# Kernel optimization log

Measured on AMD Instinct MI355X. Metric: run time of the kernel, lower is better.

## Reference

```python
import jax, jax.numpy as jnp
import numpy as np

D_MODEL, N_HEADS, WINDOW, N_STATE = 1024, 16, 256, 128
B, T = 2, 2048
EPS = 1e-5


def _layernorm(x, g, b):
    mu = jnp.mean(x, axis=-1, keepdims=True)
    var = jnp.mean((x - mu) ** 2, axis=-1, keepdims=True)
    return (x - mu) * jax.lax.rsqrt(var + EPS) * g + b


def setup_inputs() -> dict:
    key = jax.random.key(0)
    ks = jax.random.split(key, 20)
    d, h = D_MODEL, 4 * D_MODEL
    s = lambda k, *shape: jax.random.normal(k, shape, jnp.float32) * 0.02
    return {
        "x": jax.random.normal(ks[0], (B, T, d), jnp.float32),
        "ssm_state": jnp.zeros((B, N_STATE), jnp.float32),
        "ln1_g": jnp.ones((d,), jnp.float32), "ln1_b": jnp.zeros((d,), jnp.float32),
        "wq": s(ks[1], d, d), "bq": jnp.zeros((d,), jnp.float32),
        "wk": s(ks[2], d, d), "bk": jnp.zeros((d,), jnp.float32),
        "wv": s(ks[3], d, d), "bv": jnp.zeros((d,), jnp.float32),
        "wo": s(ks[4], d, d), "bo": jnp.zeros((d,), jnp.float32),
        "wg": s(ks[5], d, d), "bg": jnp.zeros((d,), jnp.float32),
        "A": jax.random.uniform(ks[6], (N_STATE,), jnp.float32, -0.1, 0.1),
        "Bw": s(ks[7], d, N_STATE),
        "Cw": s(ks[8], N_STATE, d),
        "ln2_g": jnp.ones((d,), jnp.float32), "ln2_b": jnp.zeros((d,), jnp.float32),
        "w1": s(ks[9], d, h), "b1": jnp.zeros((h,), jnp.float32),
        "w2": s(ks[10], h, d), "b2": jnp.zeros((d,), jnp.float32),
    }


def _forward(x, ssm_state, ln1_g, ln1_b, wq, bq, wk, bk, wv, bv, wo, bo,
             wg, bg, A, Bw, Cw, ln2_g, ln2_b, w1, b1, w2, b2):
    Bsz, Tlen, d = x.shape
    d_h = d // N_HEADS
    xn = _layernorm(x, ln1_g, ln1_b)

    # --- windowed causal attention (dense, per original) ---
    def heads(y):
        return y.reshape(Bsz, Tlen, N_HEADS, d_h).transpose(0, 2, 1, 3)
    Q = heads(xn @ wq + bq)
    K = heads(xn @ wk + bk)
    V = heads(xn @ wv + bv)
    scores = jnp.einsum("bhqd,bhkd->bhqk", Q, K) / (d_h ** 0.5)
    i = jnp.arange(Tlen)[:, None]
    j = jnp.arange(Tlen)[None, :]
    allowed = (j <= i) & (i - j < WINDOW)
    scores = jnp.where(allowed, scores, -jnp.inf)
    attn = jax.nn.softmax(scores, axis=-1)
    ao = jnp.einsum("bhqk,bhkd->bhqd", attn, V)
    ao = ao.transpose(0, 2, 1, 3).reshape(Bsz, Tlen, d)
    attn_out = ao @ wo + bo

    # --- diagonal SSM scan ---
    u = xn @ Bw  # (B,T,N)
    def step(s, u_t):
        s = A * s + u_t
        return s, s
    new_state, states = jax.lax.scan(step, ssm_state, u.transpose(1, 0, 2))
    ssm_out = states.transpose(1, 0, 2) @ Cw  # (B,T,d)

    # --- gated fusion + residual + MLP ---
    g = jax.nn.sigmoid(xn @ wg + bg)
    x = x + g * attn_out + (1.0 - g) * ssm_out
    xn2 = _layernorm(x, ln2_g, ln2_b)
    mlp = jax.nn.gelu(xn2 @ w1 + b1, approximate=False) @ w2 + b2
    return x + mlp, new_state


def reference(x, ssm_state, ln1_g, ln1_b, wq, bq, wk, bk, wv, bv, wo, bo,
              wg, bg, A, Bw, Cw, ln2_g, ln2_b, w1, b1, w2, b2):
    return _forward(x, ssm_state, ln1_g, ln1_b, wq, bq, wk, bk, wv, bv, wo, bo,
                    wg, bg, A, Bw, Cw, ln2_g, ln2_b, w1, b1, w2, b2)
```

## Files before the change

kernel.cpp:

```cpp
#include <hip/hip_runtime.h>

typedef __attribute__((ext_vector_type(8))) short bf16x8;
typedef __attribute__((ext_vector_type(4))) float f32x4;

#define D_MODEL 1024
#define T_LEN 2048
#define BATCH 2
#define N_HEADS 16
#define D_HEAD 64
#define WINDOW 256
#define N_STATE 128
#define D_FF 4096
#define N_CAT 4224
#define LDQ 4352
#define M_ROWS 4096

static __device__ __forceinline__ float bf2f(unsigned short u) {
  union { unsigned int i; float f; } v; v.i = ((unsigned int)u) << 16; return v.f;
}
static __device__ __forceinline__ unsigned short f2bf(float f) {
  unsigned int x = __float_as_uint(f);
  return (unsigned short)((x + 0x7FFFu + ((x >> 16) & 1u)) >> 16);
}

static __device__ __forceinline__ void gl_lds16(const void* g, void* l) {
  __builtin_amdgcn_global_load_lds(
      (const __attribute__((address_space(1))) unsigned int*)g,
      (__attribute__((address_space(3))) unsigned int*)l, 16, 0, 0);
}

__global__ __launch_bounds__(256) void transpose_cvt(
    const float* __restrict__ src, unsigned short* __restrict__ dst,
    int K, int N, int n_off, int ldd)
{
  __shared__ float tile[32][33];
  const int kt = blockIdx.x * 32, nt = blockIdx.y * 32;
  const int c = threadIdx.x & 31, r0 = threadIdx.x >> 5;
#pragma unroll
  for (int i = 0; i < 4; i++) {
    const int r = r0 + i * 8;
    tile[r][c] = src[(size_t)(kt + r) * N + nt + c];
  }
  __syncthreads();
#pragma unroll
  for (int i = 0; i < 4; i++) {
    const int r = r0 + i * 8;
    dst[(size_t)(n_off + nt + r) * ldd + kt + c] = f2bf(tile[c][r]);
  }
}

__global__ __launch_bounds__(256) void transpose5(
    const float* __restrict__ s0, const float* __restrict__ s1,
    const float* __restrict__ s2, const float* __restrict__ s3,
    const float* __restrict__ s4, unsigned short* __restrict__ dcat,
    unsigned short* __restrict__ dwo)
{
  __shared__ float tile[32][33];
  const int z = blockIdx.z;
  const float* src = (z == 0) ? s0 : (z == 1) ? s1 : (z == 2) ? s2 : (z == 3) ? s3 : s4;
  unsigned short* dst = (z < 4) ? dcat + (size_t)z * 1024 * 1024 : dwo;
  const int kt = blockIdx.x * 32, nt = blockIdx.y * 32;
  const int c = threadIdx.x & 31, r0 = threadIdx.x >> 5;
#pragma unroll
  for (int i = 0; i < 4; i++) {
    const int r = r0 + i * 8;
    tile[r][c] = src[(size_t)(kt + r) * 1024 + nt + c];
  }
  __syncthreads();
#pragma unroll
  for (int i = 0; i < 4; i++) {
    const int r = r0 + i * 8;
    dst[(size_t)(nt + r) * 1024 + kt + c] = f2bf(tile[c][r]);
  }
}

__global__ __launch_bounds__(256) void vtrans_kernel(
    const unsigned short* __restrict__ qkvgu, unsigned short* __restrict__ VT)
{
  __shared__ unsigned short tile[32][33];
  const int bh = blockIdx.z;
  const int b = bh >> 4, h = bh & 15;
  const int t0 = blockIdx.x * 32, d0 = blockIdx.y * 32;
  const int c = threadIdx.x & 31, r0 = threadIdx.x >> 5;
#pragma unroll
  for (int i = 0; i < 4; i++) {
    const int r = r0 + i * 8;
    tile[r][c] = qkvgu[((size_t)b * T_LEN + t0 + r) * LDQ + 2048 + h * 64 + d0 + c];
  }
  __syncthreads();
#pragma unroll
  for (int i = 0; i < 4; i++) {
    const int r = r0 + i * 8;
    VT[((size_t)bh * 64 + d0 + r) * T_LEN + t0 + c] = tile[c][r];
  }
}

__global__ __launch_bounds__(256) void build_bcat(
    const float* __restrict__ bq, const float* __restrict__ bk,
    const float* __restrict__ bv, const float* __restrict__ bg,
    float* __restrict__ bcat)
{
  const int i = blockIdx.x * 256 + threadIdx.x;
  if (i < LDQ) {
    float v = 0.0f;
    if (i < 1024)      v = bq[i];
    else if (i < 2048) v = bk[i - 1024];
    else if (i < 3072) v = bv[i - 2048];
    else if (i < 4096) v = bg[i - 3072];
    bcat[i] = v;
  }
}

__global__ __launch_bounds__(256) void ln_kernel(
    const float* __restrict__ x, const float* __restrict__ g,
    const float* __restrict__ b, unsigned short* __restrict__ out)
{
  const int row = blockIdx.x, tid = threadIdx.x;
  const float4 xv = ((const float4*)(x + (size_t)row * 1024))[tid];
  float s  = xv.x + xv.y + xv.z + xv.w;
  float s2 = xv.x * xv.x + xv.y * xv.y + xv.z * xv.z + xv.w * xv.w;
#pragma unroll
  for (int off = 32; off >= 1; off >>= 1) {
    s  += __shfl_down(s, off);
    s2 += __shfl_down(s2, off);
  }
  __shared__ float red[8];
  const int wave = tid >> 6;
  if ((tid & 63) == 0) { red[wave] = s; red[4 + wave] = s2; }
  __syncthreads();
  s  = red[0] + red[1] + red[2] + red[3];
  s2 = red[4] + red[5] + red[6] + red[7];
  const float mu = s * (1.0f / 1024.0f);
  const float rs = rsqrtf(s2 * (1.0f / 1024.0f) - mu * mu + 1e-5f);
  const float4 gv = ((const float4*)g)[tid];
  const float4 bv = ((const float4*)b)[tid];
  ushort4 o;
  o.x = f2bf((xv.x - mu) * rs * gv.x + bv.x);
  o.y = f2bf((xv.y - mu) * rs * gv.y + bv.y);
  o.z = f2bf((xv.z - mu) * rs * gv.z + bv.z);
  o.w = f2bf((xv.w - mu) * rs * gv.w + bv.w);
  ((ushort4*)(out + (size_t)row * 1024))[tid] = o;
}

template<int ACT>
__global__ __launch_bounds__(256, 3) void gemm128ho(
    const unsigned short* __restrict__ A, const unsigned short* __restrict__ BT,
    const float* __restrict__ bias, unsigned short* __restrict__ C,
    int ldc, int K, int nby)
{
  __shared__ char smem[32768];
  char* const As = smem;
  char* const Bs = smem + 16384;
  const int nwg = gridDim.x;
  int bid = blockIdx.x;
  {
    const int q = nwg >> 3, r = nwg & 7, xx = bid & 7, o = bid >> 3;
    bid = (xx < r ? xx * (q + 1) : r * (q + 1) + (xx - r) * q) + o;
  }
  const int per_group = 8 * nby;
  const int grp = bid / per_group, rem = bid % per_group;
  const int m0 = (grp * 8 + (rem & 7)) * 128;
  const int n0 = (rem >> 3) * 128;

  const int tid = threadIdx.x, lane = tid & 63, wave = tid >> 6;
  const int l15 = lane & 15, lg = lane >> 4;
  const int wm = (wave >> 1) * 64, wn = (wave & 1) * 64;
  f32x4 acc[4][4];
#pragma unroll
  for (int i = 0; i < 4; i++)
#pragma unroll
    for (int j = 0; j < 4; j++) acc[i][j] = (f32x4){0.f, 0.f, 0.f, 0.f};

  const char* srcA[4]; const char* srcB[4];
#pragma unroll
  for (int j = 0; j < 4; j++) {
    const int p = j * 4096 + tid * 16;
    const int R = p >> 7;
    const int cb = (p & 127) ^ ((R & 7) << 4);
    srcA[j] = (const char*)A  + (size_t)(m0 + R) * (size_t)(K * 2) + cb;
    srcB[j] = (const char*)BT + (size_t)(n0 + R) * (size_t)(K * 2) + cb;
  }

  const int NT = K >> 6;
  for (int t = 0; t < NT; ++t) {
    __syncthreads();
#pragma unroll
    for (int j = 0; j < 4; j++) {
      gl_lds16(srcA[j] + (size_t)t * 128, As + j * 4096 + tid * 16);
      gl_lds16(srcB[j] + (size_t)t * 128, Bs + j * 4096 + tid * 16);
    }
    __syncthreads();
    bf16x8 af[4][2], bfr[4][2];
#pragma unroll
    for (int mf = 0; mf < 4; mf++)
#pragma unroll
      for (int ks = 0; ks < 2; ks++) {
        const int R = wm + mf * 16 + l15;
        af[mf][ks] = *(const bf16x8*)(As + (R << 7) + ((ks * 64 + lg * 16) ^ ((R & 7) << 4)));
      }
#pragma unroll
    for (int nf = 0; nf < 4; nf++)
#pragma unroll
      for (int ks = 0; ks < 2; ks++) {
        const int R = wn + nf * 16 + l15;
        bfr[nf][ks] = *(const bf16x8*)(Bs + (R << 7) + ((ks * 64 + lg * 16) ^ ((R & 7) << 4)));
      }
#pragma unroll
    for (int mf = 0; mf < 4; mf++)
#pragma unroll
      for (int nf = 0; nf < 4; nf++)
#pragma unroll
        for (int ks = 0; ks < 2; ks++)
          acc[mf][nf] = __builtin_amdgcn_mfma_f32_16x16x32_bf16(
              af[mf][ks], bfr[nf][ks], acc[mf][nf], 0, 0, 0);
  }

  __syncthreads();
  unsigned short (*Ct)[128] = (unsigned short(*)[128])smem;
#pragma unroll
  for (int nf = 0; nf < 4; nf++) {
    const int col = wn + nf * 16 + l15;
    const float bv = bias[n0 + col];
#pragma unroll
    for (int mf = 0; mf < 4; mf++) {
      const int rbase = wm + mf * 16 + lg * 4;
#pragma unroll
      for (int r = 0; r < 4; r++) {
        float v = acc[mf][nf][r] + bv;
        if (ACT == 2) v = 0.5f * v * (1.0f + erff(v * 0.70710678118654752f));
        Ct[rbase + r][col] = f2bf(v);
      }
    }
  }
  __syncthreads();
#pragma unroll
  for (int pass = 0; pass < 8; pass++) {
    const int idx = pass * 256 + tid;
    const int row = idx >> 4, c8 = (idx & 15) * 8;
    const uint4 d = *(const uint4*)&Ct[row][c8];
    *(uint4*)(C + (size_t)(m0 + row) * ldc + n0 + c8) = d;
  }
}

template<int ACT, bool OUT_BF16, bool RESID>
__global__ __launch_bounds__(256, 4) void gemm_ho(
    const unsigned short* __restrict__ A, const unsigned short* __restrict__ BT,
    const float* __restrict__ bias, const float* __restrict__ resid,
    void* __restrict__ Cout, int ldc, int K, int nbx)
{
  __shared__ char As[16384];
  __shared__ char Bs[8192];
  const int nwg = gridDim.x;
  int bid = blockIdx.x;
  {
    const int q = nwg >> 3, r = nwg & 7, xx = bid & 7, o = bid >> 3;
    bid = (xx < r ? xx * (q + 1) : r * (q + 1) + (xx - r) * q) + o;
  }
  const int m0 = (bid % nbx) * 128;
  const int n0 = (bid / nbx) * 64;
  const int tid = threadIdx.x, lane = tid & 63, wave = tid >> 6;
  const int l15 = lane & 15, lg = lane >> 4;
  const int wm = (wave & 1) * 64, wn = (wave >> 1) * 32;
  f32x4 acc[4][2];
#pragma unroll
  for (int i = 0; i < 4; i++)
#pragma unroll
    for (int j = 0; j < 2; j++) acc[i][j] = (f32x4){0.f, 0.f, 0.f, 0.f};

  const char* srcA[4]; const char* srcB[2];
#pragma unroll
  for (int j = 0; j < 4; j++) {
    const int p = j * 4096 + tid * 16;
    const int R = p >> 7;
    const int cb = (p & 127) ^ ((R & 7) << 4);
    srcA[j] = (const char*)A + (size_t)(m0 + R) * (size_t)(K * 2) + cb;
    if (j < 2) srcB[j] = (const char*)BT + (size_t)(n0 + R) * (size_t)(K * 2) + cb;
  }

  const int NT = K >> 6;
  for (int t = 0; t < NT; ++t) {
    __syncthreads();
#pragma unroll
    for (int j = 0; j < 4; j++)
      gl_lds16(srcA[j] + (size_t)t * 128, As + j * 4096 + tid * 16);
#pragma unroll
    for (int j = 0; j < 2; j++)
      gl_lds16(srcB[j] + (size_t)t * 128, Bs + j * 4096 + tid * 16);
    __syncthreads();
    bf16x8 af[4][2], bfr[2][2];
#pragma unroll
    for (int mf = 0; mf < 4; mf++)
#pragma unroll
      for (int ks = 0; ks < 2; ks++) {
        const int R = wm + mf * 16 + l15;
        af[mf][ks] = *(const bf16x8*)(As + (R << 7) + ((ks * 64 + lg * 16) ^ ((R & 7) << 4)));
      }
#pragma unroll
    for (int nf = 0; nf < 2; nf++)
#pragma unroll
      for (int ks = 0; ks < 2; ks++) {
        const int R = wn + nf * 16 + l15;
        bfr[nf][ks] = *(const bf16x8*)(Bs + (R << 7) + ((ks * 64 + lg * 16) ^ ((R & 7) << 4)));
      }
#pragma unroll
    for (int mf = 0; mf < 4; mf++)
#pragma unroll
      for (int nf = 0; nf < 2; nf++)
#pragma unroll
        for (int ks = 0; ks < 2; ks++)
          acc[mf][nf] = __builtin_amdgcn_mfma_f32_16x16x32_bf16(
              af[mf][ks], bfr[nf][ks], acc[mf][nf], 0, 0, 0);
  }

  if (OUT_BF16) {
    __syncthreads();
    unsigned short (*Ct)[64] = (unsigned short(*)[64])As;
#pragma unroll
    for (int nf = 0; nf < 2; nf++) {
      const int col = wn + nf * 16 + l15;
      const float bv = bias ? bias[n0 + col] : 0.0f;
#pragma unroll
      for (int mf = 0; mf < 4; mf++) {
        const int rbase = wm + mf * 16 + lg * 4;
#pragma unroll
        for (int r = 0; r < 4; r++) {
          float v = acc[mf][nf][r] + bv;
          if (ACT == 2) v = 0.5f * v * (1.0f + erff(v * 0.70710678118654752f));
          Ct[rbase + r][col] = f2bf(v);
        }
      }
    }
    __syncthreads();
    unsigned short* Cb = (unsigned short*)Cout;
#pragma unroll
    for (int pass = 0; pass < 4; pass++) {
      const int idx = pass * 256 + tid;
      const int row = idx >> 3, c8 = (idx & 7) * 8;
      const uint4 d = *(const uint4*)&Ct[row][c8];
      *(uint4*)(Cb + (size_t)(m0 + row) * ldc + n0 + c8) = d;
    }
  } else {
#pragma unroll
    for (int nf = 0; nf < 2; nf++) {
      const int col = n0 + wn + nf * 16 + l15;
      const float bv = bias ? bias[col] : 0.0f;
#pragma unroll
      for (int mf = 0; mf < 4; mf++) {
        const int rbase = m0 + wm + mf * 16 + lg * 4;
#pragma unroll
        for (int r = 0; r < 4; r++) {
          float v = acc[mf][nf][r] + bv;
          if (ACT == 2) v = 0.5f * v * (1.0f + erff(v * 0.70710678118654752f));
          const size_t idx = (size_t)(rbase + r) * ldc + col;
          if (RESID) v += resid[idx];
          ((float*)Cout)[idx] = v;
        }
      }
    }
  }
}

__global__ __launch_bounds__(256) void attn_kernel(
    const unsigned short* __restrict__ qkvgu, const unsigned short* __restrict__ VT,
    unsigned short* __restrict__ ao)
{
  __shared__ float S[16][276];
  unsigned short* P = (unsigned short*)&S[0][0];

  const int bx = ((blockIdx.x & 7) << 4) | (blockIdx.x >> 3);
  const int q0 = bx * 16;
  const int h  = blockIdx.y;
  const int b  = blockIdx.z;
  const int tid = threadIdx.x, lane = tid & 63, wave = tid >> 6;
  const int l15 = lane & 15, lg = lane >> 4;
  const size_t rowbase = (size_t)b * T_LEN;

  {
    const unsigned short* qp = qkvgu + (rowbase + q0 + l15) * LDQ + h * 64 + lg * 8;
    const bf16x8 aq0 = *(const bf16x8*)qp;
    const bf16x8 aq1 = *(const bf16x8*)(qp + 32);
    for (int kt = wave; kt < 17; kt += 4) {
      const int kbase = q0 - 256 + kt * 16;
      const int krow = kbase + l15;
      const int krc = krow < 0 ? 0 : krow;
      const unsigned short* kp = qkvgu + (rowbase + krc) * LDQ + 1024 + h * 64 + lg * 8;
      const bf16x8 bk0 = *(const bf16x8*)kp;
      const bf16x8 bk1 = *(const bf16x8*)(kp + 32);
      f32x4 sacc = (f32x4){0.f, 0.f, 0.f, 0.f};
      sacc = __builtin_amdgcn_mfma_f32_16x16x32_bf16(aq0, bk0, sacc, 0, 0, 0);
      sacc = __builtin_amdgcn_mfma_f32_16x16x32_bf16(aq1, bk1, sacc, 0, 0, 0);
#pragma unroll
      for (int r = 0; r < 4; r++) {
        const int qi = q0 + lg * 4 + r;
        const int kj = kbase + l15;
        const bool ok = (kj >= 0) && (kj <= qi) && (qi - kj < WINDOW);
        S[lg * 4 + r][kt * 16 + l15] = ok ? sacc[r] * 0.125f : -1e30f;
      }
    }
  }
  __syncthreads();

  {
    const int q = tid >> 4, sub = tid & 15;
    float mx = -1e30f;
    for (int c = sub; c < 272; c += 16) mx = fmaxf(mx, S[q][c]);
#pragma unroll
    for (int off = 8; off >= 1; off >>= 1) mx = fmaxf(mx, __shfl_xor(mx, off));
    float sum = 0.f;
    for (int c = sub; c < 272; c += 16) sum += __expf(S[q][c] - mx);
#pragma unroll
    for (int off = 8; off >= 1; off >>= 1) sum += __shfl_xor(sum, off);
    const float inv = 1.0f / sum;
    unsigned short* Prow = P + q * 552;
    for (int c = sub; c < 288; c += 16) {
      const float pv = (c < 272) ? __expf(S[q][c] - mx) * inv : 0.0f;
      Prow[c] = f2bf(pv);
    }
  }
  __syncthreads();

  {
    f32x4 oacc = (f32x4){0.f, 0.f, 0.f, 0.f};
    const int dn = wave * 16 + l15;
    const unsigned short* vrow = VT + ((size_t)(b * 16 + h) * 64 + dn) * T_LEN;
#pragma unroll
    for (int ks = 0; ks < 9; ks++) {
      const bf16x8 pa = *(const bf16x8*)(P + l15 * 552 + ks * 32 + lg * 8);
      int t = q0 - 256 + ks * 32 + lg * 8;
      t = t < 0 ? 0 : (t > T_LEN - 8 ? T_LEN - 8 : t);
      const bf16x8 vb = *(const bf16x8*)(vrow + t);
      oacc = __builtin_amdgcn_mfma_f32_16x16x32_bf16(pa, vb, oacc, 0, 0, 0);
    }
#pragma unroll
    for (int r = 0; r < 4; r++)
      ao[(rowbase + q0 + lg * 4 + r) * D_MODEL + h * 64 + dn] = f2bf(oacc[r]);
  }
}

__global__ __launch_bounds__(1024) void scan_kernel(
    const unsigned short* __restrict__ qkvgu, const float* __restrict__ Avec,
    const float* __restrict__ s0, unsigned short* __restrict__ states,
    float* __restrict__ out_state)
{
  __shared__ float finals[16][128];
  const int b = blockIdx.x;
  const int tid = threadIdx.x;
  const int c = tid >> 6;
  const int n0 = (tid & 63) * 2;
  const float a0 = Avec[n0], a1 = Avec[n0 + 1];
  float sv0 = (c == 0) ? s0[b * 128 + n0]     : 0.0f;
  float sv1 = (c == 0) ? s0[b * 128 + n0 + 1] : 0.0f;
  const size_t ubase = (size_t)b * T_LEN * LDQ + 4096 + n0;
  unsigned short* sp = states + (size_t)b * T_LEN * N_STATE + n0;
  const int t0 = c * 128;
#pragma unroll 8
  for (int t = t0; t < t0 + 128; t++) {
    const ushort2 u = *(const ushort2*)&qkvgu[ubase + (size_t)t * LDQ];
    sv0 = fmaf(a0, sv0, bf2f(u.x));
    sv1 = fmaf(a1, sv1, bf2f(u.y));
    ushort2 o; o.x = f2bf(sv0); o.y = f2bf(sv1);
    *(ushort2*)&sp[(size_t)t * N_STATE] = o;
  }
  finals[c][n0] = sv0;
  finals[c][n0 + 1] = sv1;
  if (c == 15) { out_state[b * 128 + n0] = sv0; out_state[b * 128 + n0 + 1] = sv1; }
  __syncthreads();
  if (c > 0) {
    const float c0 = finals[c - 1][n0];
    const float c1 = finals[c - 1][n0 + 1];
    float f0 = a0, f1 = a1;
    for (int t = t0; t < t0 + 128; t++) {
      if (f0 == 0.0f && f1 == 0.0f) break;
      ushort2 cur = *(ushort2*)&sp[(size_t)t * N_STATE];
      cur.x = f2bf(bf2f(cur.x) + f0 * c0);
      cur.y = f2bf(bf2f(cur.y) + f1 * c1);
      *(ushort2*)&sp[(size_t)t * N_STATE] = cur;
      f0 *= a0; f1 *= a1;
    }
  }
}

__global__ __launch_bounds__(256) void fusion_ln2_kernel(
    const float* __restrict__ x, const unsigned short* __restrict__ qkvgu,
    const unsigned short* __restrict__ attn, const unsigned short* __restrict__ ssm,
    const float* __restrict__ g2, const float* __restrict__ b2,
    float* __restrict__ out, unsigned short* __restrict__ xn2)
{
  const int row = blockIdx.x, tid = threadIdx.x;
  const size_t e4 = (size_t)row * 1024 + tid * 4;
  const float4 xv = *(const float4*)(x + e4);
  const ushort4 au = *(const ushort4*)(attn + e4);
  const ushort4 su = *(const ushort4*)(ssm + e4);
  const ushort4 gu = *(const ushort4*)(qkvgu + (size_t)row * LDQ + 3072 + tid * 4);
  float4 o;
  {
    const float ga = 1.0f / (1.0f + __expf(-bf2f(gu.x)));
    const float gb = 1.0f / (1.0f + __expf(-bf2f(gu.y)));
    const float gc = 1.0f / (1.0f + __expf(-bf2f(gu.z)));
    const float gd = 1.0f / (1.0f + __expf(-bf2f(gu.w)));
    o.x = xv.x + ga * bf2f(au.x) + (1.0f - ga) * bf2f(su.x);
    o.y = xv.y + gb * bf2f(au.y) + (1.0f - gb) * bf2f(su.y);
    o.z = xv.z + gc * bf2f(au.z) + (1.0f - gc) * bf2f(su.z);
    o.w = xv.w + gd * bf2f(au.w) + (1.0f - gd) * bf2f(su.w);
  }
  *(float4*)(out + e4) = o;

  float s  = o.x + o.y + o.z + o.w;
  float s2 = o.x * o.x + o.y * o.y + o.z * o.z + o.w * o.w;
#pragma unroll
  for (int off = 32; off >= 1; off >>= 1) {
    s  += __shfl_down(s, off);
    s2 += __shfl_down(s2, off);
  }
  __shared__ float red[8];
  const int wave = tid >> 6;
  if ((tid & 63) == 0) { red[wave] = s; red[4 + wave] = s2; }
  __syncthreads();
  s  = red[0] + red[1] + red[2] + red[3];
  s2 = red[4] + red[5] + red[6] + red[7];
  const float mu = s * (1.0f / 1024.0f);
  const float rs = rsqrtf(s2 * (1.0f / 1024.0f) - mu * mu + 1e-5f);
  const float4 gv = ((const float4*)g2)[tid];
  const float4 bv = ((const float4*)b2)[tid];
  ushort4 ov;
  ov.x = f2bf((o.x - mu) * rs * gv.x + bv.x);
  ov.y = f2bf((o.y - mu) * rs * gv.y + bv.y);
  ov.z = f2bf((o.z - mu) * rs * gv.z + bv.z);
  ov.w = f2bf((o.w - mu) * rs * gv.w + bv.w);
  ((ushort4*)(xn2 + (size_t)row * 1024))[tid] = ov;
}

extern "C" void kernel_launch(void* const* d_in, const int* in_sizes, int n_in,
                              void* d_out, int out_size, void* d_ws, size_t ws_size,
                              hipStream_t stream)
{
  const float* x     = (const float*)d_in[0];
  const float* ssm0  = (const float*)d_in[1];
  const float* ln1_g = (const float*)d_in[2];
  const float* ln1_b = (const float*)d_in[3];
  const float* wq    = (const float*)d_in[4];
  const float* bq    = (const float*)d_in[5];
  const float* wk    = (const float*)d_in[6];
  const float* bk    = (const float*)d_in[7];
  const float* wv    = (const float*)d_in[8];
  const float* bv    = (const float*)d_in[9];
  const float* wo    = (const float*)d_in[10];
  const float* bo    = (const float*)d_in[11];
  const float* wg    = (const float*)d_in[12];
  const float* bg    = (const float*)d_in[13];
  const float* Av    = (const float*)d_in[14];
  const float* Bw    = (const float*)d_in[15];
  const float* Cw    = (const float*)d_in[16];
  const float* ln2_g = (const float*)d_in[17];
  const float* ln2_b = (const float*)d_in[18];
  const float* w1    = (const float*)d_in[19];
  const float* b1    = (const float*)d_in[20];
  const float* w2    = (const float*)d_in[21];
  const float* b2    = (const float*)d_in[22];

  char* p = (char*)d_ws;
  auto take = [&](size_t bytes) { char* q = p; p += (bytes + 255) & ~(size_t)255; return q; };
  unsigned short* WcatT  = (unsigned short*)take((size_t)LDQ * 1024 * 2);
  unsigned short* woT    = (unsigned short*)take((size_t)1024 * 1024 * 2);
  unsigned short* CwT    = (unsigned short*)take((size_t)1024 * 128 * 2);
  unsigned short* w1T    = (unsigned short*)take((size_t)4096 * 1024 * 2);
  unsigned short* w2T    = (unsigned short*)take((size_t)1024 * 4096 * 2);
  float*          bcat   = (float*)take((size_t)LDQ * 4);
  unsigned short* xn     = (unsigned short*)take((size_t)M_ROWS * 1024 * 2);
  unsigned short* qkvgu  = (unsigned short*)take((size_t)M_ROWS * LDQ * 2);
  unsigned short* VT     = (unsigned short*)take((size_t)BATCH * N_HEADS * 64 * T_LEN * 2);
  unsigned short* ao     = (unsigned short*)take((size_t)M_ROWS * 1024 * 2);
  unsigned short* states = (unsigned short*)take((size_t)M_ROWS * N_STATE * 2);
  unsigned short* attn_o = (unsigned short*)take((size_t)M_ROWS * 1024 * 2);
  unsigned short* ssm_o  = (unsigned short*)take((size_t)M_ROWS * 1024 * 2);
  unsigned short* hbuf   = qkvgu;

  float* outx = (float*)d_out;
  float* out_state = outx + (size_t)M_ROWS * 1024;

  transpose5<<<dim3(32, 32, 5), 256, 0, stream>>>(wq, wk, wv, wg, wo, WcatT, woT);
  transpose_cvt<<<dim3(32, 4), 256, 0, stream>>>(Bw, WcatT, 1024, 128, 4096, 1024);
  transpose_cvt<<<dim3(4, 32), 256, 0, stream>>>(Cw, CwT, 128, 1024, 0, 128);
  transpose_cvt<<<dim3(32, 128), 256, 0, stream>>>(w1, w1T, 1024, 4096, 0, 1024);
  transpose_cvt<<<dim3(128, 32), 256, 0, stream>>>(w2, w2T, 4096, 1024, 0, 4096);
  build_bcat<<<17, 256, 0, stream>>>(bq, bk, bv, bg, bcat);

  ln_kernel<<<M_ROWS, 256, 0, stream>>>(x, ln1_g, ln1_b, xn);
  gemm128ho<0><<<32 * 34, 256, 0, stream>>>(xn, WcatT, bcat, qkvgu, LDQ, 1024, 34);
  vtrans_kernel<<<dim3(64, 2, 32), 256, 0, stream>>>(qkvgu, VT);
  attn_kernel<<<dim3(128, 16, 2), 256, 0, stream>>>(qkvgu, VT, ao);
  scan_kernel<<<2, 1024, 0, stream>>>(qkvgu, Av, ssm0, states, out_state);
  gemm_ho<0, true, false><<<32 * 16, 256, 0, stream>>>(
      ao, woT, bo, nullptr, attn_o, 1024, 1024, 32);
  gemm_ho<0, true, false><<<32 * 16, 256, 0, stream>>>(
      states, CwT, nullptr, nullptr, ssm_o, 1024, 128, 32);
  fusion_ln2_kernel<<<4096, 256, 0, stream>>>(
      x, qkvgu, attn_o, ssm_o, ln2_g, ln2_b, outx, xn);
  gemm128ho<2><<<32 * 32, 256, 0, stream>>>(xn, w1T, b1, hbuf, 4096, 1024, 32);
  gemm_ho<0, false, true><<<32 * 16, 256, 0, stream>>>(
      hbuf, w2T, b2, outx, outx, 1024, 4096, 32);
}
```

Measured before the change: 307.7 us.

## Merge prep kernels, fold scan into attention launch, dual-job output GEMM

Replaces the six weight-transpose and bias-concat launches with a single prep kernel indexed by a flat block id. Folds the SSM scan into extra blocks of the attention launch, using four 512-step chunks per batch instead of sixteen 128-step chunks, so it overlaps with attention. Replaces the two separate output-projection and Cw GEMMs with one launch using 128x64 tiles that serves both jobs. Also raises the occupancy hint of gemm128ho. Fewer launches and more concurrency are the goal, but the scan now has a longer serial chain per thread and occupies only two blocks.

```diff
diff --git a/kernel.cpp b/kernel.cpp
--- a/kernel.cpp
+++ b/kernel.cpp
@@ -29,12 +29,55 @@
       (__attribute__((address_space(3))) unsigned int*)l, 16, 0, 0);
 }
 
-__global__ __launch_bounds__(256) void transpose_cvt(
-    const float* __restrict__ src, unsigned short* __restrict__ dst,
-    int K, int N, int n_off, int ldd)
-{
+__global__ __launch_bounds__(256) void prep_kernel(
+    const float* __restrict__ wq, const float* __restrict__ wk,
+    const float* __restrict__ wv, const float* __restrict__ wg,
+    const float* __restrict__ wo, const float* __restrict__ Bw,
+    const float* __restrict__ Cw, const float* __restrict__ w1,
+    const float* __restrict__ w2,
+    const float* __restrict__ bq, const float* __restrict__ bk,
+    const float* __restrict__ bv, const float* __restrict__ bg,
+    unsigned short* __restrict__ WcatT, unsigned short* __restrict__ woT,
+    unsigned short* __restrict__ CwT, unsigned short* __restrict__ w1T,
+    unsigned short* __restrict__ w2T, float* __restrict__ bcat)
+{
+  const int bid = blockIdx.x;
+  if (bid >= 13568) {
+    const int i = (bid - 13568) * 256 + threadIdx.x;
+    if (i < LDQ) {
+      float v = 0.0f;
+      if (i < 1024)      v = bq[i];
+      else if (i < 2048) v = bk[i - 1024];
+      else if (i < 3072) v = bv[i - 2048];
+      else if (i < 4096) v = bg[i - 3072];
+      bcat[i] = v;
+    }
+    return;
+  }
+  const float* src; unsigned short* dst;
+  int N, n_off, ldd, x, y;
+  if (bid < 5120) {
+    const int z = bid >> 10, t = bid & 1023;
+    x = t & 31; y = t >> 5;
+    src = (z == 0) ? wq : (z == 1) ? wk : (z == 2) ? wv : (z == 3) ? wg : wo;
+    dst = (z < 4) ? WcatT : woT;
+    n_off = (z < 4) ? z * 1024 : 0;
+    N = 1024; ldd = 1024;
+  } else if (bid < 5248) {
+    const int t = bid - 5120; x = t & 31; y = t >> 5;
+    src = Bw; dst = WcatT; n_off = 4096; N = 128; ldd = 1024;
+  } else if (bid < 5376) {
+    const int t = bid - 5248; x = t & 3; y = t >> 2;
+    src = Cw; dst = CwT; n_off = 0; N = 1024; ldd = 128;
+  } else if (bid < 9472) {
+    const int t = bid - 5376; x = t & 31; y = t >> 5;
+    src = w1; dst = w1T; n_off = 0; N = 4096; ldd = 1024;
+  } else {
+    const int t = bid - 9472; x = t & 127; y = t >> 7;
+    src = w2; dst = w2T; n_off = 0; N = 1024; ldd = 4096;
+  }
   __shared__ float tile[32][33];
-  const int kt = blockIdx.x * 32, nt = blockIdx.y * 32;
+  const int kt = x * 32, nt = y * 32;
   const int c = threadIdx.x & 31, r0 = threadIdx.x >> 5;
 #pragma unroll
   for (int i = 0; i < 4; i++) {
@@ -46,31 +89,6 @@
   for (int i = 0; i < 4; i++) {
     const int r = r0 + i * 8;
     dst[(size_t)(n_off + nt + r) * ldd + kt + c] = f2bf(tile[c][r]);
-  }
-}
-
-__global__ __launch_bounds__(256) void transpose5(
-    const float* __restrict__ s0, const float* __restrict__ s1,
-    const float* __restrict__ s2, const float* __restrict__ s3,
-    const float* __restrict__ s4, unsigned short* __restrict__ dcat,
-    unsigned short* __restrict__ dwo)
-{
-  __shared__ float tile[32][33];
-  const int z = blockIdx.z;
-  const float* src = (z == 0) ? s0 : (z == 1) ? s1 : (z == 2) ? s2 : (z == 3) ? s3 : s4;
-  unsigned short* dst = (z < 4) ? dcat + (size_t)z * 1024 * 1024 : dwo;
-  const int kt = blockIdx.x * 32, nt = blockIdx.y * 32;
-  const int c = threadIdx.x & 31, r0 = threadIdx.x >> 5;
-#pragma unroll
-  for (int i = 0; i < 4; i++) {
-    const int r = r0 + i * 8;
-    tile[r][c] = src[(size_t)(kt + r) * 1024 + nt + c];
-  }
-  __syncthreads();
-#pragma unroll
-  for (int i = 0; i < 4; i++) {
-    const int r = r0 + i * 8;
-    dst[(size_t)(nt + r) * 1024 + kt + c] = f2bf(tile[c][r]);
   }
 }
 
@@ -92,22 +110,6 @@
   for (int i = 0; i < 4; i++) {
     const int r = r0 + i * 8;
     VT[((size_t)bh * 64 + d0 + r) * T_LEN + t0 + c] = tile[c][r];
-  }
-}
-
-__global__ __launch_bounds__(256) void build_bcat(
-    const float* __restrict__ bq, const float* __restrict__ bk,
-    const float* __restrict__ bv, const float* __restrict__ bg,
-    float* __restrict__ bcat)
-{
-  const int i = blockIdx.x * 256 + threadIdx.x;
-  if (i < LDQ) {
-    float v = 0.0f;
-    if (i < 1024)      v = bq[i];
-    else if (i < 2048) v = bk[i - 1024];
-    else if (i < 3072) v = bv[i - 2048];
-    else if (i < 4096) v = bg[i - 3072];
-    bcat[i] = v;
   }
 }
 
@@ -143,7 +145,7 @@
 }
 
 template<int ACT>
-__global__ __launch_bounds__(256, 3) void gemm128ho(
+__global__ __launch_bounds__(256, 4) void gemm128ho(
     const unsigned short* __restrict__ A, const unsigned short* __restrict__ BT,
     const float* __restrict__ bias, unsigned short* __restrict__ C,
     int ldc, int K, int nby)
@@ -360,18 +362,164 @@
   }
 }
 
-__global__ __launch_bounds__(256) void attn_kernel(
+__global__ __launch_bounds__(256, 4) void gemm_dual(
+    const unsigned short* __restrict__ A1, const unsigned short* __restrict__ BT1,
+    const float* __restrict__ bias1, unsigned short* __restrict__ C1, int K1,
+    const unsigned short* __restrict__ A2, const unsigned short* __restrict__ BT2,
+    const float* __restrict__ bias2, unsigned short* __restrict__ C2, int K2)
+{
+  __shared__ char As[16384];
+  __shared__ char Bs[8192];
+  const int nwg = gridDim.x;
+  int bid = blockIdx.x;
+  {
+    const int q = nwg >> 3, r = nwg & 7, xx = bid & 7, o = bid >> 3;
+    bid = (xx < r ? xx * (q + 1) : r * (q + 1) + (xx - r) * q) + o;
+  }
+  const int job = bid >> 9;
+  const int inner = bid & 511;
+  const unsigned short* A  = job ? A2 : A1;
+  const unsigned short* BT = job ? BT2 : BT1;
+  const float* bias        = job ? bias2 : bias1;
+  unsigned short* C        = job ? C2 : C1;
+  const int K              = job ? K2 : K1;
+  const int m0 = (inner & 31) * 128;
+  const int n0 = (inner >> 5) * 64;
+  const int ldc = 1024;
+
+  const int tid = threadIdx.x, lane = tid & 63, wave = tid >> 6;
+  const int l15 = lane & 15, lg = lane >> 4;
+  const int wm = (wave & 1) * 64, wn = (wave >> 1) * 32;
+  f32x4 acc[4][2];
+#pragma unroll
+  for (int i = 0; i < 4; i++)
+#pragma unroll
+    for (int j = 0; j < 2; j++) acc[i][j] = (f32x4){0.f, 0.f, 0.f, 0.f};
+
+  const char* srcA[4]; const char* srcB[2];
+#pragma unroll
+  for (int j = 0; j < 4; j++) {
+    const int p = j * 4096 + tid * 16;
+    const int R = p >> 7;
+    const int cb = (p & 127) ^ ((R & 7) << 4);
+    srcA[j] = (const char*)A + (size_t)(m0 + R) * (size_t)(K * 2) + cb;
+    if (j < 2) srcB[j] = (const char*)BT + (size_t)(n0 + R) * (size_t)(K * 2) + cb;
+  }
+
+  const int NT = K >> 6;
+  for (int t = 0; t < NT; ++t) {
+    __syncthreads();
+#pragma unroll
+    for (int j = 0; j < 4; j++)
+      gl_lds16(srcA[j] + (size_t)t * 128, As + j * 4096 + tid * 16);
+#pragma unroll
+    for (int j = 0; j < 2; j++)
+      gl_lds16(srcB[j] + (size_t)t * 128, Bs + j * 4096 + tid * 16);
+    __syncthreads();
+    bf16x8 af[4][2], bfr[2][2];
+#pragma unroll
+    for (int mf = 0; mf < 4; mf++)
+#pragma unroll
+      for (int ks = 0; ks < 2; ks++) {
+        const int R = wm + mf * 16 + l15;
+        af[mf][ks] = *(const bf16x8*)(As + (R << 7) + ((ks * 64 + lg * 16) ^ ((R & 7) << 4)));
+      }
+#pragma unroll
+    for (int nf = 0; nf < 2; nf++)
+#pragma unroll
+      for (int ks = 0; ks < 2; ks++) {
+        const int R = wn + nf * 16 + l15;
+        bfr[nf][ks] = *(const bf16x8*)(Bs + (R << 7) + ((ks * 64 + lg * 16) ^ ((R & 7) << 4)));
+      }
+#pragma unroll
+    for (int mf = 0; mf < 4; mf++)
+#pragma unroll
+      for (int nf = 0; nf < 2; nf++)
+#pragma unroll
+        for (int ks = 0; ks < 2; ks++)
+          acc[mf][nf] = __builtin_amdgcn_mfma_f32_16x16x32_bf16(
+              af[mf][ks], bfr[nf][ks], acc[mf][nf], 0, 0, 0);
+  }
+
+  __syncthreads();
+  unsigned short (*Ct)[64] = (unsigned short(*)[64])As;
+#pragma unroll
+  for (int nf = 0; nf < 2; nf++) {
+    const int col = wn + nf * 16 + l15;
+    const float bv = bias ? bias[n0 + col] : 0.0f;
+#pragma unroll
+    for (int mf = 0; mf < 4; mf++) {
+      const int rbase = wm + mf * 16 + lg * 4;
+#pragma unroll
+      for (int r = 0; r < 4; r++)
+        Ct[rbase + r][col] = f2bf(acc[mf][nf][r] + bv);
+    }
+  }
+  __syncthreads();
+#pragma unroll
+  for (int pass = 0; pass < 4; pass++) {
+    const int idx = pass * 256 + tid;
+    const int row = idx >> 3, c8 = (idx & 7) * 8;
+    const uint4 d = *(const uint4*)&Ct[row][c8];
+    *(uint4*)(C + (size_t)(m0 + row) * ldc + n0 + c8) = d;
+  }
+}
+
+__global__ __launch_bounds__(256) void attn_scan_kernel(
     const unsigned short* __restrict__ qkvgu, const unsigned short* __restrict__ VT,
-    unsigned short* __restrict__ ao)
+    unsigned short* __restrict__ ao, const float* __restrict__ Avec,
+    const float* __restrict__ s0, unsigned short* __restrict__ states,
+    float* __restrict__ out_state)
 {
   __shared__ float S[16][276];
+  const int tid = threadIdx.x;
+
+  if (blockIdx.x >= 128) {
+    if (blockIdx.y != 0 || blockIdx.z != 0 || blockIdx.x > 129) return;
+    float (*finals)[128] = (float(*)[128])&S[0][0];
+    const int b = blockIdx.x - 128;
+    const int c = tid >> 6;
+    const int n0 = (tid & 63) * 2;
+    const float a0 = Avec[n0], a1 = Avec[n0 + 1];
+    float sv0 = (c == 0) ? s0[b * 128 + n0]     : 0.0f;
+    float sv1 = (c == 0) ? s0[b * 128 + n0 + 1] : 0.0f;
+    const size_t ubase = (size_t)b * T_LEN * LDQ + 4096 + n0;
+    unsigned short* sp = states + (size_t)b * T_LEN * N_STATE + n0;
+    const int t0 = c * 512;
+#pragma unroll 8
+    for (int t = t0; t < t0 + 512; t++) {
+      const ushort2 u = *(const ushort2*)&qkvgu[ubase + (size_t)t * LDQ];
+      sv0 = fmaf(a0, sv0, bf2f(u.x));
+      sv1 = fmaf(a1, sv1, bf2f(u.y));
+      ushort2 o; o.x = f2bf(sv0); o.y = f2bf(sv1);
+      *(ushort2*)&sp[(size_t)t * N_STATE] = o;
+    }
+    finals[c][n0] = sv0;
+    finals[c][n0 + 1] = sv1;
+    if (c == 3) { out_state[b * 128 + n0] = sv0; out_state[b * 128 + n0 + 1] = sv1; }
+    __syncthreads();
+    if (c > 0) {
+      const float c0 = finals[c - 1][n0];
+      const float c1 = finals[c - 1][n0 + 1];
+      float f0 = a0, f1 = a1;
+      for (int t = t0; t < t0 + 512; t++) {
+        if (f0 == 0.0f && f1 == 0.0f) break;
+        ushort2 cur = *(ushort2*)&sp[(size_t)t * N_STATE];
+        cur.x = f2bf(bf2f(cur.x) + f0 * c0);
+        cur.y = f2bf(bf2f(cur.y) + f1 * c1);
+        *(ushort2*)&sp[(size_t)t * N_STATE] = cur;
+        f0 *= a0; f1 *= a1;
+      }
+    }
+    return;
+  }
+
   unsigned short* P = (unsigned short*)&S[0][0];
-
   const int bx = ((blockIdx.x & 7) << 4) | (blockIdx.x >> 3);
   const int q0 = bx * 16;
   const int h  = blockIdx.y;
   const int b  = blockIdx.z;
-  const int tid = threadIdx.x, lane = tid & 63, wave = tid >> 6;
+  const int lane = tid & 63, wave = tid >> 6;
   const int l15 = lane & 15, lg = lane >> 4;
   const size_t rowbase = (size_t)b * T_LEN;
 
@@ -434,49 +582,6 @@
 #pragma unroll
     for (int r = 0; r < 4; r++)
       ao[(rowbase + q0 + lg * 4 + r) * D_MODEL + h * 64 + dn] = f2bf(oacc[r]);
-  }
-}
-
-__global__ __launch_bounds__(1024) void scan_kernel(
-    const unsigned short* __restrict__ qkvgu, const float* __restrict__ Avec,
-    const float* __restrict__ s0, unsigned short* __restrict__ states,
-    float* __restrict__ out_state)
-{
-  __shared__ float finals[16][128];
-  const int b = blockIdx.x;
-  const int tid = threadIdx.x;
-  const int c = tid >> 6;
-  const int n0 = (tid & 63) * 2;
-  const float a0 = Avec[n0], a1 = Avec[n0 + 1];
-  float sv0 = (c == 0) ? s0[b * 128 + n0]     : 0.0f;
-  float sv1 = (c == 0) ? s0[b * 128 + n0 + 1] : 0.0f;
-  const size_t ubase = (size_t)b * T_LEN * LDQ + 4096 + n0;
-  unsigned short* sp = states + (size_t)b * T_LEN * N_STATE + n0;
-  const int t0 = c * 128;
-#pragma unroll 8
-  for (int t = t0; t < t0 + 128; t++) {
-    const ushort2 u = *(const ushort2*)&qkvgu[ubase + (size_t)t * LDQ];
-    sv0 = fmaf(a0, sv0, bf2f(u.x));
-    sv1 = fmaf(a1, sv1, bf2f(u.y));
-    ushort2 o; o.x = f2bf(sv0); o.y = f2bf(sv1);
-    *(ushort2*)&sp[(size_t)t * N_STATE] = o;
-  }
-  finals[c][n0] = sv0;
-  finals[c][n0 + 1] = sv1;
-  if (c == 15) { out_state[b * 128 + n0] = sv0; out_state[b * 128 + n0 + 1] = sv1; }
-  __syncthreads();
-  if (c > 0) {
-    const float c0 = finals[c - 1][n0];
-    const float c1 = finals[c - 1][n0 + 1];
-    float f0 = a0, f1 = a1;
-    for (int t = t0; t < t0 + 128; t++) {
-      if (f0 == 0.0f && f1 == 0.0f) break;
-      ushort2 cur = *(ushort2*)&sp[(size_t)t * N_STATE];
-      cur.x = f2bf(bf2f(cur.x) + f0 * c0);
-      cur.y = f2bf(bf2f(cur.y) + f1 * c1);
-      *(ushort2*)&sp[(size_t)t * N_STATE] = cur;
-      f0 *= a0; f1 *= a1;
-    }
   }
 }
 
@@ -578,22 +683,18 @@
   float* outx = (float*)d_out;
   float* out_state = outx + (size_t)M_ROWS * 1024;
 
-  transpose5<<<dim3(32, 32, 5), 256, 0, stream>>>(wq, wk, wv, wg, wo, WcatT, woT);
-  transpose_cvt<<<dim3(32, 4), 256, 0, stream>>>(Bw, WcatT, 1024, 128, 4096, 1024);
-  transpose_cvt<<<dim3(4, 32), 256, 0, stream>>>(Cw, CwT, 128, 1024, 0, 128);
-  transpose_cvt<<<dim3(32, 128), 256, 0, stream>>>(w1, w1T, 1024, 4096, 0, 1024);
-  transpose_cvt<<<dim3(128, 32), 256, 0, stream>>>(w2, w2T, 4096, 1024, 0, 4096);
-  build_bcat<<<17, 256, 0, stream>>>(bq, bk, bv, bg, bcat);
+  prep_kernel<<<13585, 256, 0, stream>>>(
+      wq, wk, wv, wg, wo, Bw, Cw, w1, w2, bq, bk, bv, bg,
+      WcatT, woT, CwT, w1T, w2T, bcat);
 
   ln_kernel<<<M_ROWS, 256, 0, stream>>>(x, ln1_g, ln1_b, xn);
   gemm128ho<0><<<32 * 34, 256, 0, stream>>>(xn, WcatT, bcat, qkvgu, LDQ, 1024, 34);
   vtrans_kernel<<<dim3(64, 2, 32), 256, 0, stream>>>(qkvgu, VT);
-  attn_kernel<<<dim3(128, 16, 2), 256, 0, stream>>>(qkvgu, VT, ao);
-  scan_kernel<<<2, 1024, 0, stream>>>(qkvgu, Av, ssm0, states, out_state);
-  gemm_ho<0, true, false><<<32 * 16, 256, 0, stream>>>(
-      ao, woT, bo, nullptr, attn_o, 1024, 1024, 32);
-  gemm_ho<0, true, false><<<32 * 16, 256, 0, stream>>>(
-      states, CwT, nullptr, nullptr, ssm_o, 1024, 128, 32);
+  attn_scan_kernel<<<dim3(130, 16, 2), 256, 0, stream>>>(
+      qkvgu, VT, ao, Av, ssm0, states, out_state);
+  gemm_dual<<<1024, 256, 0, stream>>>(
+      ao, woT, bo, attn_o, 1024,
+      states, CwT, nullptr, ssm_o, 128);
   fusion_ln2_kernel<<<4096, 256, 0, stream>>>(
       x, qkvgu, attn_o, ssm_o, ln2_g, ln2_b, outx, xn);
   gemm128ho<2><<<32 * 32, 256, 0, stream>>>(xn, w1T, b1, hbuf, 4096, 1024, 32);
```

Result: faster. 296.4 us (-3.6%).
